# Kernel optimization log

Hardware: AMD Instinct MI355X
Metric: run time of the kernel (lower is better)

Reference implementation:

```python
import jax, jax.numpy as jnp
import numpy as np

T, D = 256, 256
N, F, DM, H1, H2 = T + D, 2048, 512, 128, 64
E_HALF = T * D            # edges with src < dst (track -> detection)
LAM, SLACK = 5.0, -0.2    # hardcoded in original forward
SINK_ITERS = 8


def setup_inputs() -> dict:
    key = jax.random.key(0)
    ks = jax.random.split(key, 16)
    x = jax.random.normal(ks[0], (N, F), jnp.float32)
    coords = jax.random.normal(ks[1], (N, 4), jnp.float32)
    # boxes in xyxy with positive extent for IoU
    c = jax.random.uniform(ks[2], (N, 2), jnp.float32) * 0.8
    wh = jax.random.uniform(ks[3], (N, 2), jnp.float32) * 0.2 + 0.01
    coords_original = jnp.concatenate([c, c + wh], axis=1)
    ground_truth = (jax.random.uniform(ks[4], (E_HALF,)) < 0.1).astype(jnp.float32)
    # full bipartite directed edges: first half track->det (src<dst), second half reversed
    t = jnp.arange(T, dtype=jnp.int32)
    d = jnp.arange(D, dtype=jnp.int32) + T
    src_h = jnp.repeat(t, D)
    dst_h = jnp.tile(d, T)
    edge_index = jnp.stack([jnp.concatenate([src_h, dst_h]),
                            jnp.concatenate([dst_h, src_h])])

    def w(k, shape, fan_in):
        return jax.random.normal(k, shape, jnp.float32) / np.sqrt(fan_in).astype(np.float32)

    params = dict(
        W_enc=w(ks[5], (F, DM), F), b_enc=jnp.zeros((DM,), jnp.float32),
        app_W1=w(ks[6], (2 * DM, H1), 2 * DM), app_b1=jnp.zeros((H1,), jnp.float32),
        app_w2=w(ks[7], (H1,), H1), app_b2=jnp.zeros((), jnp.float32),
        geo_W1=w(ks[8], (8, H2), 8), geo_b1=jnp.zeros((H2,), jnp.float32),
        geo_w2=w(ks[9], (H2,), H2), geo_b2=jnp.zeros((), jnp.float32),
        aff_w=w(ks[10], (2,), 2), aff_b=jnp.zeros((), jnp.float32),
        W_self=w(ks[11], (DM, DM), DM), W_nbr=w(ks[12], (DM, DM), DM),
        b_mp=jnp.zeros((DM,), jnp.float32),
        fin_w=w(ks[13], (2,), 2), fin_b=jnp.zeros((), jnp.float32),
    )
    return dict(x=x, coords=coords, coords_original=coords_original,
                ground_truth=ground_truth, edge_index=edge_index, **params)


def _box_iou(a, b):
    # a, b: [E, 4] xyxy boxes
    lt = jnp.maximum(a[:, :2], b[:, :2])
    rb = jnp.minimum(a[:, 2:], b[:, 2:])
    wh = jnp.clip(rb - lt, 0.0)
    inter = wh[:, 0] * wh[:, 1]
    area_a = (a[:, 2] - a[:, 0]) * (a[:, 3] - a[:, 1])
    area_b = (b[:, 2] - b[:, 0]) * (b[:, 3] - b[:, 1])
    return inter / (area_a + area_b - inter + 1e-6)


def _forward(x, coords, coords_original, edge_index,
             W_enc, b_enc, app_W1, app_b1, app_w2, app_b2,
             geo_W1, geo_b1, geo_w2, geo_b2, aff_w, aff_b,
             W_self, W_nbr, b_mp, fin_w, fin_b):
    src, dst = edge_index[0], edge_index[1]
    # EncoderCNN -> node embeddings [N, DM]
    h = jax.nn.relu(x @ W_enc + b_enc)
    hs, hd = h[src], h[dst]                       # per-edge gathers [E, DM]
    # appearance affinity MLP on concat embeddings -> scalar per edge
    x1 = jax.nn.sigmoid(jax.nn.relu(jnp.concatenate([hs, hd], 1) @ app_W1 + app_b1) @ app_w2 + app_b2)
    # geometric affinity MLP on concat coords -> scalar per edge
    geo = jnp.concatenate([coords[src], coords[dst]], 1)   # [E, 8]
    x2 = jax.nn.sigmoid(jax.nn.relu(geo @ geo_W1 + geo_b1) @ geo_w2 + geo_b2)
    iou = _box_iou(coords_original[src], coords_original[dst])   # [E]
    # combine -> edge weight (affinityNet)
    ew = jax.nn.sigmoid(jnp.stack([x1, x2], axis=-1) @ aff_w + aff_b)  # [E]
    # optimNet: weighted message passing -> updated node embeddings
    agg = jax.ops.segment_sum(ew[:, None] * (hs @ W_nbr), dst, num_segments=N)
    out = jax.nn.relu(h @ W_self + agg + b_mp)    # [N, DM]
    # edges with src < dst are exactly the first E_HALF by construction
    a, b = out[src[:E_HALF]], out[dst[:E_HALF]]
    na = jnp.clip(jnp.linalg.norm(a, axis=1), 1e-6)
    nb = jnp.clip(jnp.linalg.norm(b, axis=1), 1e-6)
    cos = jnp.sum(a * b, axis=1) / (na * nb)
    fin = jax.nn.sigmoid(jnp.stack([cos, iou[:E_HALF]], axis=-1) @ fin_w + fin_b)  # [E_HALF]
    # scatter-built cost matrix with slack row/column, Sinkhorn normalization
    sv = jnp.exp(jnp.float32(SLACK * LAM))
    M = jnp.zeros((T + 1, D + 1), jnp.float32)
    M = M.at[src[:E_HALF], dst[:E_HALF] - T].set(jnp.exp(fin * LAM))
    M = M.at[:, D].set(sv)
    M = M.at[T, :].set(sv)
    for _ in range(SINK_ITERS):
        M = M / jnp.sum(M, axis=1, keepdims=True)
        M = M / jnp.sum(M, axis=0, keepdims=True)
    return M[:T, :D].reshape(-1)   # [T*D]


def reference(x, coords, coords_original, ground_truth, edge_index,
              W_enc, b_enc, app_W1, app_b1, app_w2, app_b2,
              geo_W1, geo_b1, geo_w2, geo_b2, aff_w, aff_b,
              W_self, W_nbr, b_mp, fin_w, fin_b):
    normalized = _forward(x, coords, coords_original, edge_index,
                          W_enc, b_enc, app_W1, app_b1, app_w2, app_b2,
                          geo_W1, geo_b1, geo_w2, geo_b2, aff_w, aff_b,
                          W_self, W_nbr, b_mp, fin_w, fin_b)
    # post-Sinkhorn entries are strictly positive, so the !=0 filter is identity
    det_num = jnp.full((1,), D, jnp.int32)
    tracklet_num = jnp.full((1,), T, jnp.int32)
    return normalized, ground_truth, det_num, tracklet_num
```

## Files before the change

kernel.cpp:

```cpp
#include <hip/hip_runtime.h>
#include <hip/hip_fp16.h>
#include <math.h>

#define EH   65536
#define LAMF 5.0f
#define SVF  0.36787944117144233f

typedef __bf16 bf16x8 __attribute__((ext_vector_type(8)));
typedef float  f32x4  __attribute__((ext_vector_type(4)));
typedef _Float16 f16x2 __attribute__((ext_vector_type(2)));

__device__ __forceinline__ float sigmoidf_(float x) { return 1.0f / (1.0f + expf(-x)); }

__device__ __forceinline__ void cvt1(float v, ushort& h, ushort& l) {
    __bf16 bh = (__bf16)v;
    h = __builtin_bit_cast(ushort, bh);
    __bf16 bl = (__bf16)(v - (float)bh);
    l = __builtin_bit_cast(ushort, bl);
}

__device__ __forceinline__ f16x2 u2h(uint u) { return __builtin_bit_cast(f16x2, u); }

#define LSTR 40
template<int MODE>
__global__ __launch_bounds__(256) void gemm64(
    const float* __restrict__ Aa, const float* __restrict__ Ab,
    const float* __restrict__ B0, const float* __restrict__ B1,
    const float* __restrict__ B2,
    const float* __restrict__ HsC45, const float* __restrict__ bmp,
    float* __restrict__ C0, float* __restrict__ C1)
{
    __shared__ ushort As_hi[64*LSTR], As_lo[64*LSTR], Bs_hi[64*LSTR], Bs_lo[64*LSTR];
    const int tid = threadIdx.x;
    const int row0 = blockIdx.y * 64;

    const float* Ap = Aa; int lda, arow0 = row0, ak = 0;
    const float* Bp; int ldb, kb = 0, bcol0;
    float* Cp; int ldc, ccol0;
    int KS;

    if (MODE == 0) {
        KS = 512; lda = 2048; ak = blockIdx.z * 512;
        Bp = B0; ldb = 512; kb = blockIdx.z * 512; bcol0 = blockIdx.x * 64;
        Cp = C0 + blockIdx.z * 262144; ldc = 512; ccol0 = bcol0;
    } else if (MODE == 1) {
        KS = 512; lda = 512;
        int cb = blockIdx.x;
        if (cb < 8)       { Bp=B0; ldb=512; kb=0;   bcol0=cb*64;        Cp=C0; ldc=1024; ccol0=cb*64; }
        else if (cb < 16) { Bp=B1; ldb=512; kb=0;   bcol0=(cb-8)*64;    Cp=C0; ldc=1024; ccol0=512+(cb-8)*64; }
        else if (cb < 18) { Bp=B2; ldb=128; kb=0;   bcol0=(cb-16)*64;   Cp=C1; ldc=256;  ccol0=(cb-16)*64; }
        else              { Bp=B2; ldb=128; kb=512; bcol0=(cb-18)*64;   Cp=C1; ldc=256;  ccol0=128+(cb-18)*64; }
    } else {
        KS = 256; lda = 256;
        if (row0 < 256) { Ap = Aa; arow0 = row0;       kb = 256; }
        else            { Ap = Ab; arow0 = row0 - 256; kb = 0; }
        Bp = B0; ldb = 1024; bcol0 = blockIdx.x * 64;
        Cp = C0; ldc = 512; ccol0 = bcol0;
    }

    const int arow = tid >> 2, kq = (tid & 3) * 8;
    const int kr = (tid & 15) * 2, nc0 = (tid >> 4) * 4;
    const float* aptr = Ap + (size_t)(arow0 + arow) * lda + ak + kq;
    const float* bptr = Bp + (size_t)(kb + kr) * ldb + bcol0 + nc0;

    f32x4 acc[2][2] = {};
    const int lane = tid & 63, w = tid >> 6;
    const int qr = (w >> 1) * 32, qc = (w & 1) * 32;
    const int fr = lane & 15, kg = (lane >> 4) * 8;

    float4 pa0, pa1, pb0, pb1;
    pa0 = *(const float4*)aptr; pa1 = *(const float4*)(aptr + 4);
    pb0 = *(const float4*)bptr; pb1 = *(const float4*)(bptr + ldb);

    for (int k0 = 0; k0 < KS; k0 += 32) {
        {
            ushort4 h0, l0, h1, l1;
            cvt1(pa0.x,h0.x,l0.x); cvt1(pa0.y,h0.y,l0.y); cvt1(pa0.z,h0.z,l0.z); cvt1(pa0.w,h0.w,l0.w);
            cvt1(pa1.x,h1.x,l1.x); cvt1(pa1.y,h1.y,l1.y); cvt1(pa1.z,h1.z,l1.z); cvt1(pa1.w,h1.w,l1.w);
            *(ushort4*)&As_hi[arow*LSTR + kq]     = h0;
            *(ushort4*)&As_hi[arow*LSTR + kq + 4] = h1;
            *(ushort4*)&As_lo[arow*LSTR + kq]     = l0;
            *(ushort4*)&As_lo[arow*LSTR + kq + 4] = l1;
            float b0a[4] = {pb0.x, pb0.y, pb0.z, pb0.w};
            float b1a[4] = {pb1.x, pb1.y, pb1.z, pb1.w};
            #pragma unroll
            for (int j = 0; j < 4; ++j) {
                ushort ha, la, hb, lb;
                cvt1(b0a[j], ha, la); cvt1(b1a[j], hb, lb);
                *(uint*)&Bs_hi[(nc0+j)*LSTR + kr] = (uint)ha | ((uint)hb << 16);
                *(uint*)&Bs_lo[(nc0+j)*LSTR + kr] = (uint)la | ((uint)lb << 16);
            }
        }
        __syncthreads();
        if (k0 + 32 < KS) {
            pa0 = *(const float4*)(aptr + k0 + 32);
            pa1 = *(const float4*)(aptr + k0 + 36);
            const float* bp2 = bptr + (size_t)(k0 + 32) * ldb;
            pb0 = *(const float4*)bp2; pb1 = *(const float4*)(bp2 + ldb);
        }
        bf16x8 ah[2], al[2], bh[2], bl[2];
        #pragma unroll
        for (int m = 0; m < 2; ++m) {
            int r = (qr + m*16 + fr) * LSTR + kg;
            ah[m] = *(const bf16x8*)&As_hi[r];
            al[m] = *(const bf16x8*)&As_lo[r];
        }
        #pragma unroll
        for (int n = 0; n < 2; ++n) {
            int r = (qc + n*16 + fr) * LSTR + kg;
            bh[n] = *(const bf16x8*)&Bs_hi[r];
            bl[n] = *(const bf16x8*)&Bs_lo[r];
        }
        #pragma unroll
        for (int m = 0; m < 2; ++m)
            #pragma unroll
            for (int n = 0; n < 2; ++n) {
                acc[m][n] = __builtin_amdgcn_mfma_f32_16x16x32_bf16(ah[m], bh[n], acc[m][n], 0, 0, 0);
                acc[m][n] = __builtin_amdgcn_mfma_f32_16x16x32_bf16(ah[m], bl[n], acc[m][n], 0, 0, 0);
                acc[m][n] = __builtin_amdgcn_mfma_f32_16x16x32_bf16(al[m], bh[n], acc[m][n], 0, 0, 0);
            }
        __syncthreads();
    }

    const int rbase = (lane >> 4) * 4;
    #pragma unroll
    for (int m = 0; m < 2; ++m)
        #pragma unroll
        for (int n = 0; n < 2; ++n)
            #pragma unroll
            for (int r = 0; r < 4; ++r) {
                int gr = row0 + qr + m*16 + rbase + r;
                int gc = ccol0 + qc + n*16 + (lane & 15);
                float v = acc[m][n][r];
                if (MODE == 2) {
                    v += HsC45[(size_t)gr * 1024 + 512 + gc] + bmp[gc];
                    v = fmaxf(v, 0.f);
                }
                Cp[(size_t)gr * ldc + gc] = v;
            }
}

__global__ __launch_bounds__(256) void enc_reduce(const float* __restrict__ P,
    const float* __restrict__ bias, float* __restrict__ h)
{
    int e = (blockIdx.x * 256 + threadIdx.x) * 4;
    int col = e & 511;
    float4 v0 = *(const float4*)&P[e];
    float4 v1 = *(const float4*)&P[e + 262144];
    float4 v2 = *(const float4*)&P[e + 524288];
    float4 v3 = *(const float4*)&P[e + 786432];
    float4 b  = *(const float4*)&bias[col];
    float4 o;
    o.x = fmaxf(v0.x + v1.x + v2.x + v3.x + b.x, 0.f);
    o.y = fmaxf(v0.y + v1.y + v2.y + v3.y + b.y, 0.f);
    o.z = fmaxf(v0.z + v1.z + v2.z + v3.z + b.z, 0.f);
    o.w = fmaxf(v0.w + v1.w + v2.w + v3.w + b.w, 0.f);
    *(float4*)&h[e] = o;
}

__global__ __launch_bounds__(256) void edge_geo_kernel(
    const float* __restrict__ C23, const float* __restrict__ coords,
    const float* __restrict__ geo_W1, const float* __restrict__ geo_b1,
    const float* __restrict__ app_b1, const float* __restrict__ app_w2,
    const float* __restrict__ app_b2, const float* __restrict__ geo_w2,
    const float* __restrict__ geo_b2, const float* __restrict__ aff_w,
    const float* __restrict__ aff_b, const float* __restrict__ co,
    float* __restrict__ ewT0, float* __restrict__ ew2, float* __restrict__ iou1)
{
    __shared__ float sA[16][129], sB[16][129], sGA[16][65], sGB[16][65];
    __shared__ float sw2[128], sb1[128], sgw2[64];
    __shared__ float sgw[8][64], sgb[64], scs[16][4], scd[16][4];
    const int tid = threadIdx.x;
    const int half = blockIdx.z;
    const int t0 = blockIdx.y * 16, d0 = blockIdx.x * 16;
    const int sbase = half ? (256 + d0) : t0;
    const int dbase = half ? t0 : (256 + d0);
    for (int i = tid; i < 16 * 32; i += 256) {
        int rr = i >> 5, c4 = (i & 31) << 2;
        float4 va = *(const float4*)&C23[(sbase + rr) * 256 + c4];
        sA[rr][c4] = va.x; sA[rr][c4+1] = va.y; sA[rr][c4+2] = va.z; sA[rr][c4+3] = va.w;
        float4 vb = *(const float4*)&C23[(dbase + rr) * 256 + 128 + c4];
        sB[rr][c4] = vb.x; sB[rr][c4+1] = vb.y; sB[rr][c4+2] = vb.z; sB[rr][c4+3] = vb.w;
    }
    for (int i = tid; i < 512; i += 256) sgw[i >> 6][i & 63] = geo_W1[i];
    if (tid < 64) sgb[tid] = geo_b1[tid];
    else if (tid < 192) { sw2[tid-64] = app_w2[tid-64]; sb1[tid-64] = app_b1[tid-64]; }
    else { sgw2[tid - 192] = geo_w2[tid - 192]; }
    if (tid < 64) scs[tid >> 2][tid & 3] = coords[(sbase + (tid >> 2)) * 4 + (tid & 3)];
    else if (tid < 128) { int i = tid - 64; scd[i >> 2][i & 3] = coords[(dbase + (i >> 2)) * 4 + (i & 3)]; }
    __syncthreads();
    for (int v = tid; v < 2048; v += 256) {
        int hh = v >> 10, rr = (v >> 6) & 15, j = v & 63;
        if (hh == 0) {
            sGA[rr][j] = scs[rr][0]*sgw[0][j] + scs[rr][1]*sgw[1][j]
                       + scs[rr][2]*sgw[2][j] + scs[rr][3]*sgw[3][j] + sgb[j];
        } else {
            sGB[rr][j] = scd[rr][0]*sgw[4][j] + scd[rr][1]*sgw[5][j]
                       + scd[rr][2]*sgw[6][j] + scd[rr][3]*sgw[7][j];
        }
    }
    __syncthreads();
    const int tx = tid & 15, ty = tid >> 4;
    const int si = half ? tx : ty;
    const int di = half ? ty : tx;
    float acc1 = 0.f;
    #pragma unroll 8
    for (int j = 0; j < 128; ++j) {
        float v = sA[si][j] + sB[di][j] + sb1[j];
        acc1 += fmaxf(v, 0.f) * sw2[j];
    }
    float x1 = sigmoidf_(acc1 + app_b2[0]);
    float acc2 = 0.f;
    #pragma unroll 8
    for (int j = 0; j < 64; ++j) {
        float v = sGA[si][j] + sGB[di][j];
        acc2 += fmaxf(v, 0.f) * sgw2[j];
    }
    float x2 = sigmoidf_(acc2 + geo_b2[0]);
    float e = sigmoidf_(x1 * aff_w[0] + x2 * aff_w[1] + aff_b[0]);
    const int t = t0 + ty, d = d0 + tx;
    if (half) ew2[t * 256 + d] = e;
    else      ewT0[d * 256 + t] = e;
    if (half == 0) {
        float4 a = *(const float4*)&co[t * 4];
        float4 b = *(const float4*)&co[(256 + d) * 4];
        float ltx = fmaxf(a.x, b.x), lty = fmaxf(a.y, b.y);
        float rbx = fminf(a.z, b.z), rby = fminf(a.w, b.w);
        float w  = fmaxf(rbx - ltx, 0.f), hh = fmaxf(rby - lty, 0.f);
        float inter = w * hh;
        float areaA = (a.z - a.x) * (a.w - a.y);
        float areaB = (b.z - b.x) * (b.w - b.y);
        iou1[t * 256 + d] = inter / (areaA + areaB - inter + 1e-6f);
    }
}

__global__ __launch_bounds__(256) void gram32(const float* __restrict__ outm,
    const float* __restrict__ iou, const float* __restrict__ finw,
    const float* __restrict__ finb, __half* __restrict__ Mh)
{
    __shared__ ushort As_hi[32*LSTR], As_lo[32*LSTR], Bs_hi[32*LSTR], Bs_lo[32*LSTR];
    __shared__ float snA[32], snB[32];
    const int tid = threadIdx.x;
    const int t0 = blockIdx.y * 32, d0 = blockIdx.x * 32;
    const float* Asrc = outm;
    const float* Bsrc = outm + (size_t)256 * 512;

    const int arow = tid >> 3, kq = (tid & 7) * 4;
    const float* aptr = Asrc + (size_t)(t0 + arow) * 512 + kq;
    const float* bptr = Bsrc + (size_t)(d0 + arow) * 512 + kq;

    f32x4 acc = {};
    float ssA = 0.f, ssB = 0.f;
    const int lane = tid & 63, w = tid >> 6;
    const int qr = (w >> 1) * 16, qc = (w & 1) * 16;
    const int fr = lane & 15, kg = (lane >> 4) * 8;

    float4 pa = *(const float4*)aptr;
    float4 pb = *(const float4*)bptr;

    for (int k0 = 0; k0 < 512; k0 += 32) {
        ssA += pa.x*pa.x + pa.y*pa.y + pa.z*pa.z + pa.w*pa.w;
        ssB += pb.x*pb.x + pb.y*pb.y + pb.z*pb.z + pb.w*pb.w;
        {
            ushort4 h4, l4;
            cvt1(pa.x,h4.x,l4.x); cvt1(pa.y,h4.y,l4.y); cvt1(pa.z,h4.z,l4.z); cvt1(pa.w,h4.w,l4.w);
            *(ushort4*)&As_hi[arow*LSTR + kq] = h4;
            *(ushort4*)&As_lo[arow*LSTR + kq] = l4;
            cvt1(pb.x,h4.x,l4.x); cvt1(pb.y,h4.y,l4.y); cvt1(pb.z,h4.z,l4.z); cvt1(pb.w,h4.w,l4.w);
            *(ushort4*)&Bs_hi[arow*LSTR + kq] = h4;
            *(ushort4*)&Bs_lo[arow*LSTR + kq] = l4;
        }
        __syncthreads();
        if (k0 + 32 < 512) {
            pa = *(const float4*)(aptr + k0 + 32);
            pb = *(const float4*)(bptr + k0 + 32);
        }
        bf16x8 ah, al, bh, bl;
        {
            int r = (qr + fr) * LSTR + kg;
            ah = *(const bf16x8*)&As_hi[r]; al = *(const bf16x8*)&As_lo[r];
        }
        {
            int r = (qc + fr) * LSTR + kg;
            bh = *(const bf16x8*)&Bs_hi[r]; bl = *(const bf16x8*)&Bs_lo[r];
        }
        acc = __builtin_amdgcn_mfma_f32_16x16x32_bf16(ah, bh, acc, 0, 0, 0);
        acc = __builtin_amdgcn_mfma_f32_16x16x32_bf16(ah, bl, acc, 0, 0, 0);
        acc = __builtin_amdgcn_mfma_f32_16x16x32_bf16(al, bh, acc, 0, 0, 0);
        __syncthreads();
    }
    ssA += __shfl_xor(ssA, 1); ssA += __shfl_xor(ssA, 2); ssA += __shfl_xor(ssA, 4);
    ssB += __shfl_xor(ssB, 1); ssB += __shfl_xor(ssB, 2); ssB += __shfl_xor(ssB, 4);
    if ((tid & 7) == 0) { snA[arow] = ssA; snB[arow] = ssB; }
    __syncthreads();
    const float fw0 = finw[0], fw1 = finw[1], fb = finb[0];
    const int rbase = (lane >> 4) * 4, lc = qc + (lane & 15);
    #pragma unroll
    for (int r = 0; r < 4; ++r) {
        int lr = qr + rbase + r;
        float na = fmaxf(sqrtf(snA[lr]), 1e-6f);
        float nb = fmaxf(sqrtf(snB[lc]), 1e-6f);
        int t = t0 + lr, d = d0 + lc;
        float cosv = acc[r] / (na * nb);
        float fin = sigmoidf_(cosv * fw0 + iou[t * 256 + d] * fw1 + fb);
        Mh[t * 256 + d] = __float2half(expf(fin * LAMF));
    }
}

__global__ __launch_bounds__(1024, 4) void sinkhorn4(const __half* __restrict__ Mh,
    float* __restrict__ gr, float* __restrict__ gc)
{
    __shared__ float r_f[256], c_f[256], red[16];
    __shared__ __half r_h[256], c_h[256];
    const int tid = threadIdx.x;
    const int row = tid >> 2, sub4 = tid & 3;
    const int cg = tid >> 5, sub32 = tid & 31;

    const uint4* gm = (const uint4*)Mh;
    uint4 mr[8];
    #pragma unroll
    for (int j = 0; j < 8; ++j) mr[j] = gm[row * 32 + sub4 * 8 + j];
    uint4 mca[4], mcb[4];
    #pragma unroll
    for (int p = 0; p < 4; ++p) {
        int rp = 2 * sub32 + 64 * p;
        mca[p] = gm[rp * 32 + cg];
        mcb[p] = gm[(rp + 1) * 32 + cg];
    }
    if (tid < 256) { c_f[tid] = 1.0f; c_h[tid] = __float2half(1.0f); }
    if (tid == 0) red[1] = 1.0f / SVF;
    __syncthreads();

    const int b4 = (sub32 >> 4) & 1, b3 = (sub32 >> 3) & 1, b2 = (sub32 >> 2) & 1;

    for (int it = 0; it < 8; ++it) {
        float c256 = 1.0f / (SVF * red[1]);
        float a0 = 0.f, a1 = 0.f, a2 = 0.f, a3 = 0.f;
        {
            uint4 cu[4];
            #pragma unroll
            for (int j = 0; j < 4; ++j) cu[j] = *(const uint4*)&c_h[sub4 * 64 + j * 8];
            #pragma unroll
            for (int j = 0; j < 4; ++j) {
                a0 = __builtin_amdgcn_fdot2(u2h(mr[j].x), u2h(cu[j].x), a0, false);
                a1 = __builtin_amdgcn_fdot2(u2h(mr[j].y), u2h(cu[j].y), a1, false);
                a2 = __builtin_amdgcn_fdot2(u2h(mr[j].z), u2h(cu[j].z), a2, false);
                a3 = __builtin_amdgcn_fdot2(u2h(mr[j].w), u2h(cu[j].w), a3, false);
            }
            #pragma unroll
            for (int j = 0; j < 4; ++j) cu[j] = *(const uint4*)&c_h[sub4 * 64 + 32 + j * 8];
            #pragma unroll
            for (int j = 0; j < 4; ++j) {
                a0 = __builtin_amdgcn_fdot2(u2h(mr[4+j].x), u2h(cu[j].x), a0, false);
                a1 = __builtin_amdgcn_fdot2(u2h(mr[4+j].y), u2h(cu[j].y), a1, false);
                a2 = __builtin_amdgcn_fdot2(u2h(mr[4+j].z), u2h(cu[j].z), a2, false);
                a3 = __builtin_amdgcn_fdot2(u2h(mr[4+j].w), u2h(cu[j].w), a3, false);
            }
        }
        float acc = (a0 + a1) + (a2 + a3);
        acc += __shfl_xor(acc, 1); acc += __shfl_xor(acc, 2);
        if (tid < 64) {
            float s = c_f[tid] + c_f[tid + 64] + c_f[tid + 128] + c_f[tid + 192];
            #pragma unroll
            for (int o = 32; o; o >>= 1) s += __shfl_down(s, o);
            if (tid == 0) red[0] = s + c256;
        }
        if (sub4 == 0) {
            float v = 1.0f / (acc + SVF * c256);
            r_f[row] = v; r_h[row] = __float2half(v);
        }
        __syncthreads();

        float r256 = 1.0f / (SVF * red[0]);
        float b[8] = {0.f,0.f,0.f,0.f,0.f,0.f,0.f,0.f};
        #pragma unroll
        for (int p = 0; p < 4; ++p) {
            f16x2 rp = u2h(*(const uint*)&r_h[2 * sub32 + 64 * p]);
            uint lo, hi;
            lo = __builtin_amdgcn_perm(mcb[p].x, mca[p].x, 0x05040100);
            hi = __builtin_amdgcn_perm(mcb[p].x, mca[p].x, 0x07060302);
            b[0] = __builtin_amdgcn_fdot2(u2h(lo), rp, b[0], false);
            b[1] = __builtin_amdgcn_fdot2(u2h(hi), rp, b[1], false);
            lo = __builtin_amdgcn_perm(mcb[p].y, mca[p].y, 0x05040100);
            hi = __builtin_amdgcn_perm(mcb[p].y, mca[p].y, 0x07060302);
            b[2] = __builtin_amdgcn_fdot2(u2h(lo), rp, b[2], false);
            b[3] = __builtin_amdgcn_fdot2(u2h(hi), rp, b[3], false);
            lo = __builtin_amdgcn_perm(mcb[p].z, mca[p].z, 0x05040100);
            hi = __builtin_amdgcn_perm(mcb[p].z, mca[p].z, 0x07060302);
            b[4] = __builtin_amdgcn_fdot2(u2h(lo), rp, b[4], false);
            b[5] = __builtin_amdgcn_fdot2(u2h(hi), rp, b[5], false);
            lo = __builtin_amdgcn_perm(mcb[p].w, mca[p].w, 0x05040100);
            hi = __builtin_amdgcn_perm(mcb[p].w, mca[p].w, 0x07060302);
            b[6] = __builtin_amdgcn_fdot2(u2h(lo), rp, b[6], false);
            b[7] = __builtin_amdgcn_fdot2(u2h(hi), rp, b[7], false);
        }
        float t0v, t1v, t2v, t3v;
        t0v = b4 ? b[0] : b[4]; t1v = b4 ? b[1] : b[5];
        t2v = b4 ? b[2] : b[6]; t3v = b4 ? b[3] : b[7];
        t0v = __shfl_xor(t0v, 16); t1v = __shfl_xor(t1v, 16);
        t2v = __shfl_xor(t2v, 16); t3v = __shfl_xor(t3v, 16);
        float k0 = (b4 ? b[4] : b[0]) + t0v;
        float k1 = (b4 ? b[5] : b[1]) + t1v;
        float k2 = (b4 ? b[6] : b[2]) + t2v;
        float k3 = (b4 ? b[7] : b[3]) + t3v;
        float u0 = b3 ? k0 : k2, u1 = b3 ? k1 : k3;
        u0 = __shfl_xor(u0, 8); u1 = __shfl_xor(u1, 8);
        float m0 = (b3 ? k2 : k0) + u0;
        float m1 = (b3 ? k3 : k1) + u1;
        float w0 = b2 ? m0 : m1;
        w0 = __shfl_xor(w0, 4);
        float s = (b2 ? m1 : m0) + w0;
        s += __shfl_xor(s, 1); s += __shfl_xor(s, 2);
        if (tid < 64) {
            float s2 = r_f[tid] + r_f[tid + 64] + r_f[tid + 128] + r_f[tid + 192];
            #pragma unroll
            for (int o = 32; o; o >>= 1) s2 += __shfl_down(s2, o);
            if (tid == 0) red[1] = s2 + r256;
        }
        if ((sub32 & 3) == 0) {
            int col = cg * 8 + b4 * 4 + b3 * 2 + b2;
            float v = 1.0f / (s + SVF * r256);
            c_f[col] = v; c_h[col] = __float2half(v);
        }
        __syncthreads();
    }
    if (tid < 256) { gr[tid] = r_f[tid]; gc[tid] = c_f[tid]; }
}

__global__ __launch_bounds__(256) void final_kernel(const __half* __restrict__ Mh,
    const float* __restrict__ r, const float* __restrict__ c,
    const float* __restrict__ gt, float* __restrict__ out)
{
    const int bid = blockIdx.x, tid = threadIdx.x;
    if (bid < 256) {
        int k = bid * 256 + tid;
        out[k] = __half2float(Mh[k]) * r[bid] * c[tid];
    } else if (bid < 512) {
        int k = (bid - 256) * 256 + tid;
        out[EH + k] = gt[k];
    } else if (tid == 0) {
        out[2 * EH]     = 256.0f;
        out[2 * EH + 1] = 256.0f;
    }
}

extern "C" void kernel_launch(void* const* d_in, const int* in_sizes, int n_in,
                              void* d_out, int out_size, void* d_ws, size_t ws_size,
                              hipStream_t stream)
{
    const float* x       = (const float*)d_in[0];
    const float* coords  = (const float*)d_in[1];
    const float* co      = (const float*)d_in[2];
    const float* gt      = (const float*)d_in[3];
    const float* W_enc   = (const float*)d_in[5];
    const float* b_enc   = (const float*)d_in[6];
    const float* app_W1  = (const float*)d_in[7];
    const float* app_b1  = (const float*)d_in[8];
    const float* app_w2  = (const float*)d_in[9];
    const float* app_b2  = (const float*)d_in[10];
    const float* geo_W1  = (const float*)d_in[11];
    const float* geo_b1  = (const float*)d_in[12];
    const float* geo_w2  = (const float*)d_in[13];
    const float* geo_b2  = (const float*)d_in[14];
    const float* aff_w   = (const float*)d_in[15];
    const float* aff_b   = (const float*)d_in[16];
    const float* W_self  = (const float*)d_in[17];
    const float* W_nbr   = (const float*)d_in[18];
    const float* b_mp    = (const float*)d_in[19];
    const float* fin_w   = (const float*)d_in[20];
    const float* fin_b   = (const float*)d_in[21];
    float* out = (float*)d_out;

    char* W = (char*)d_ws;
    float*  P     = (float*)(W + 0);
    float*  h     = (float*)(W + 4849664);
    float*  C45   = (float*)(W + 0);
    float*  C23   = (float*)(W + 2097152);
    float*  ewT0  = (float*)(W + 2621440);
    float*  ew2   = (float*)(W + 2883584);
    float*  iou1  = (float*)(W + 3145728);
    __half* Mh    = (__half*)(W + 3407872);
    float*  grv   = (float*)(W + 3538944);
    float*  gcv   = (float*)(W + 3543040);
    float*  outm  = (float*)(W + 3670016);

    gemm64<0><<<dim3(8, 8, 4), 256, 0, stream>>>(x, nullptr, W_enc, nullptr, nullptr,
        nullptr, nullptr, P, nullptr);
    enc_reduce<<<256, 256, 0, stream>>>(P, b_enc, h);
    gemm64<1><<<dim3(20, 8), 256, 0, stream>>>(h, nullptr, W_nbr, W_self, app_W1,
        nullptr, nullptr, C45, C23);
    edge_geo_kernel<<<dim3(16, 16, 2), 256, 0, stream>>>(C23, coords, geo_W1, geo_b1,
        app_b1, app_w2, app_b2, geo_w2, geo_b2, aff_w, aff_b, co, ewT0, ew2, iou1);
    gemm64<2><<<dim3(8, 8), 256, 0, stream>>>(ew2, ewT0, C45, nullptr, nullptr,
        C45, b_mp, outm, nullptr);
    gram32<<<dim3(8, 8), 256, 0, stream>>>(outm, iou1, fin_w, fin_b, Mh);
    sinkhorn4<<<1, 1024, 0, stream>>>(Mh, grv, gcv);
    final_kernel<<<513, 256, 0, stream>>>(Mh, grv, gcv, gt, out);
}
```

Before: 90.88 us.

## Deepen encoder split-K, vectorise edge MLP loops, move gt copy into edge kernel

The encoder GEMM now splits K eight ways instead of four, giving 512 blocks, and the reduce kernel sums eight partials. The edge kernel folds app_b1 into the staged sB tile, pads its shared arrays for 16-byte alignment and reads them as float4. It also takes over the ground-truth copy and the count writes from final_kernel, which shrinks to 256 blocks. The partial buffer doubles in size and h moves to a higher workspace offset, so the extra reduce traffic may cancel the gain from more GEMM parallelism.

```diff
diff --git a/kernel.cpp b/kernel.cpp
--- a/kernel.cpp
+++ b/kernel.cpp
@@ -40,8 +40,8 @@
     int KS;
 
     if (MODE == 0) {
-        KS = 512; lda = 2048; ak = blockIdx.z * 512;
-        Bp = B0; ldb = 512; kb = blockIdx.z * 512; bcol0 = blockIdx.x * 64;
+        KS = 256; lda = 2048; ak = blockIdx.z * 256;
+        Bp = B0; ldb = 512; kb = blockIdx.z * 256; bcol0 = blockIdx.x * 64;
         Cp = C0 + blockIdx.z * 262144; ldc = 512; ccol0 = bcol0;
     } else if (MODE == 1) {
         KS = 512; lda = 512;
@@ -145,16 +145,18 @@
 {
     int e = (blockIdx.x * 256 + threadIdx.x) * 4;
     int col = e & 511;
-    float4 v0 = *(const float4*)&P[e];
-    float4 v1 = *(const float4*)&P[e + 262144];
-    float4 v2 = *(const float4*)&P[e + 524288];
-    float4 v3 = *(const float4*)&P[e + 786432];
-    float4 b  = *(const float4*)&bias[col];
+    float4 s = *(const float4*)&P[e];
+    #pragma unroll
+    for (int z = 1; z < 8; ++z) {
+        float4 v = *(const float4*)&P[e + z * 262144];
+        s.x += v.x; s.y += v.y; s.z += v.z; s.w += v.w;
+    }
+    float4 b = *(const float4*)&bias[col];
     float4 o;
-    o.x = fmaxf(v0.x + v1.x + v2.x + v3.x + b.x, 0.f);
-    o.y = fmaxf(v0.y + v1.y + v2.y + v3.y + b.y, 0.f);
-    o.z = fmaxf(v0.z + v1.z + v2.z + v3.z + b.z, 0.f);
-    o.w = fmaxf(v0.w + v1.w + v2.w + v3.w + b.w, 0.f);
+    o.x = fmaxf(s.x + b.x, 0.f);
+    o.y = fmaxf(s.y + b.y, 0.f);
+    o.z = fmaxf(s.z + b.z, 0.f);
+    o.w = fmaxf(s.w + b.w, 0.f);
     *(float4*)&h[e] = o;
 }
 
@@ -165,27 +167,44 @@
     const float* __restrict__ app_b2, const float* __restrict__ geo_w2,
     const float* __restrict__ geo_b2, const float* __restrict__ aff_w,
     const float* __restrict__ aff_b, const float* __restrict__ co,
+    const float* __restrict__ gt, float* __restrict__ outp,
     float* __restrict__ ewT0, float* __restrict__ ew2, float* __restrict__ iou1)
 {
-    __shared__ float sA[16][129], sB[16][129], sGA[16][65], sGB[16][65];
-    __shared__ float sw2[128], sb1[128], sgw2[64];
+    __shared__ __align__(16) float sA[16][132], sB[16][132];
+    __shared__ __align__(16) float sGA[16][68], sGB[16][68];
+    __shared__ __align__(16) float sw2[128], sgw2[64];
     __shared__ float sgw[8][64], sgb[64], scs[16][4], scd[16][4];
     const int tid = threadIdx.x;
     const int half = blockIdx.z;
     const int t0 = blockIdx.y * 16, d0 = blockIdx.x * 16;
     const int sbase = half ? (256 + d0) : t0;
     const int dbase = half ? t0 : (256 + d0);
+
+    if (half == 1) {
+        int bid = blockIdx.y * 16 + blockIdx.x;
+        if (tid < 64) {
+            int o = bid * 256 + tid * 4;
+            *(float4*)&outp[EH + o] = *(const float4*)&gt[o];
+        }
+        if (bid == 0 && tid == 64) {
+            outp[2 * EH]     = 256.0f;
+            outp[2 * EH + 1] = 256.0f;
+        }
+    }
+
     for (int i = tid; i < 16 * 32; i += 256) {
         int rr = i >> 5, c4 = (i & 31) << 2;
         float4 va = *(const float4*)&C23[(sbase + rr) * 256 + c4];
         sA[rr][c4] = va.x; sA[rr][c4+1] = va.y; sA[rr][c4+2] = va.z; sA[rr][c4+3] = va.w;
         float4 vb = *(const float4*)&C23[(dbase + rr) * 256 + 128 + c4];
-        sB[rr][c4] = vb.x; sB[rr][c4+1] = vb.y; sB[rr][c4+2] = vb.z; sB[rr][c4+3] = vb.w;
+        float4 b1 = *(const float4*)&app_b1[c4];
+        sB[rr][c4] = vb.x + b1.x; sB[rr][c4+1] = vb.y + b1.y;
+        sB[rr][c4+2] = vb.z + b1.z; sB[rr][c4+3] = vb.w + b1.w;
     }
     for (int i = tid; i < 512; i += 256) sgw[i >> 6][i & 63] = geo_W1[i];
     if (tid < 64) sgb[tid] = geo_b1[tid];
-    else if (tid < 192) { sw2[tid-64] = app_w2[tid-64]; sb1[tid-64] = app_b1[tid-64]; }
-    else { sgw2[tid - 192] = geo_w2[tid - 192]; }
+    else if (tid < 192) sw2[tid - 64] = app_w2[tid - 64];
+    else sgw2[tid - 192] = geo_w2[tid - 192];
     if (tid < 64) scs[tid >> 2][tid & 3] = coords[(sbase + (tid >> 2)) * 4 + (tid & 3)];
     else if (tid < 128) { int i = tid - 64; scd[i >> 2][i & 3] = coords[(dbase + (i >> 2)) * 4 + (i & 3)]; }
     __syncthreads();
@@ -204,17 +223,23 @@
     const int si = half ? tx : ty;
     const int di = half ? ty : tx;
     float acc1 = 0.f;
-    #pragma unroll 8
-    for (int j = 0; j < 128; ++j) {
-        float v = sA[si][j] + sB[di][j] + sb1[j];
-        acc1 += fmaxf(v, 0.f) * sw2[j];
+    #pragma unroll
+    for (int j4 = 0; j4 < 128; j4 += 4) {
+        float4 a = *(const float4*)&sA[si][j4];
+        float4 b = *(const float4*)&sB[di][j4];
+        float4 wv = *(const float4*)&sw2[j4];
+        acc1 += fmaxf(a.x + b.x, 0.f) * wv.x + fmaxf(a.y + b.y, 0.f) * wv.y
+              + fmaxf(a.z + b.z, 0.f) * wv.z + fmaxf(a.w + b.w, 0.f) * wv.w;
     }
     float x1 = sigmoidf_(acc1 + app_b2[0]);
     float acc2 = 0.f;
-    #pragma unroll 8
-    for (int j = 0; j < 64; ++j) {
-        float v = sGA[si][j] + sGB[di][j];
-        acc2 += fmaxf(v, 0.f) * sgw2[j];
+    #pragma unroll
+    for (int j4 = 0; j4 < 64; j4 += 4) {
+        float4 a = *(const float4*)&sGA[si][j4];
+        float4 b = *(const float4*)&sGB[di][j4];
+        float4 wv = *(const float4*)&sgw2[j4];
+        acc2 += fmaxf(a.x + b.x, 0.f) * wv.x + fmaxf(a.y + b.y, 0.f) * wv.y
+              + fmaxf(a.z + b.z, 0.f) * wv.z + fmaxf(a.w + b.w, 0.f) * wv.w;
     }
     float x2 = sigmoidf_(acc2 + geo_b2[0]);
     float e = sigmoidf_(x1 * aff_w[0] + x2 * aff_w[1] + aff_b[0]);
@@ -429,19 +454,11 @@
 
 __global__ __launch_bounds__(256) void final_kernel(const __half* __restrict__ Mh,
     const float* __restrict__ r, const float* __restrict__ c,
-    const float* __restrict__ gt, float* __restrict__ out)
+    float* __restrict__ out)
 {
     const int bid = blockIdx.x, tid = threadIdx.x;
-    if (bid < 256) {
-        int k = bid * 256 + tid;
-        out[k] = __half2float(Mh[k]) * r[bid] * c[tid];
-    } else if (bid < 512) {
-        int k = (bid - 256) * 256 + tid;
-        out[EH + k] = gt[k];
-    } else if (tid == 0) {
-        out[2 * EH]     = 256.0f;
-        out[2 * EH + 1] = 256.0f;
-    }
+    int k = bid * 256 + tid;
+    out[k] = __half2float(Mh[k]) * r[bid] * c[tid];
 }
 
 extern "C" void kernel_launch(void* const* d_in, const int* in_sizes, int n_in,
@@ -473,7 +490,7 @@
 
     char* W = (char*)d_ws;
     float*  P     = (float*)(W + 0);
-    float*  h     = (float*)(W + 4849664);
+    float*  h     = (float*)(W + 8388608);
     float*  C45   = (float*)(W + 0);
     float*  C23   = (float*)(W + 2097152);
     float*  ewT0  = (float*)(W + 2621440);
@@ -484,16 +501,17 @@
     float*  gcv   = (float*)(W + 3543040);
     float*  outm  = (float*)(W + 3670016);
 
-    gemm64<0><<<dim3(8, 8, 4), 256, 0, stream>>>(x, nullptr, W_enc, nullptr, nullptr,
+    gemm64<0><<<dim3(8, 8, 8), 256, 0, stream>>>(x, nullptr, W_enc, nullptr, nullptr,
         nullptr, nullptr, P, nullptr);
     enc_reduce<<<256, 256, 0, stream>>>(P, b_enc, h);
     gemm64<1><<<dim3(20, 8), 256, 0, stream>>>(h, nullptr, W_nbr, W_self, app_W1,
         nullptr, nullptr, C45, C23);
     edge_geo_kernel<<<dim3(16, 16, 2), 256, 0, stream>>>(C23, coords, geo_W1, geo_b1,
-        app_b1, app_w2, app_b2, geo_w2, geo_b2, aff_w, aff_b, co, ewT0, ew2, iou1);
+        app_b1, app_w2, app_b2, geo_w2, geo_b2, aff_w, aff_b, co, gt, out,
+        ewT0, ew2, iou1);
     gemm64<2><<<dim3(8, 8), 256, 0, stream>>>(ew2, ewT0, C45, nullptr, nullptr,
         C45, b_mp, outm, nullptr);
     gram32<<<dim3(8, 8), 256, 0, stream>>>(outm, iou1, fin_w, fin_b, Mh);
     sinkhorn4<<<1, 1024, 0, stream>>>(Mh, grv, gcv);
-    final_kernel<<<513, 256, 0, stream>>>(Mh, grv, gcv, gt, out);
-}
+    final_kernel<<<256, 256, 0, stream>>>(Mh, grv, gcv, out);
+}
```

New measurement: 83.81 us. -7.8%, faster.
